# Optimization experiments

Hardware: AMD Instinct MI355X
Metric: run time of the kernel (lower is better)

## Reference

```python
import jax, jax.numpy as jnp
import numpy as np

N = 64   # SSM state size
H = 256  # channels
B = 8    # batch
L = 1024 # sequence length


def setup_inputs() -> dict:
    key = jax.random.key(0)
    k1, k2, k3, k4, k5 = jax.random.split(key, 5)
    scale = 1.0 / np.sqrt(N)  # lecun_normal std for fan_in=N
    inp = jax.random.normal(k1, (B, L, H), jnp.float32)
    As = jax.random.normal(k2, (H, N, N), jnp.float32) * scale
    Bs = jax.random.normal(k3, (H, N, 1), jnp.float32) * scale
    Cs = jax.random.normal(k4, (H, 1, N), jnp.float32) * scale
    Ds = jnp.ones((H,), jnp.float32)
    # log_step_initializer: uniform in [log(dt_min), log(dt_max)]
    lo, hi = np.log(0.001), np.log(0.003)
    log_steps = jax.random.uniform(k5, (H,), jnp.float32) * (hi - lo) + lo
    return {"inp": inp, "As": As, "Bs": Bs, "Cs": Cs, "Ds": Ds, "log_steps": log_steps}


def _discretize(A, B_, C, step):
    # Bilinear (Tustin) discretization, batched over H. step: (H,)
    I = jnp.eye(A.shape[-1], dtype=A.dtype)
    s = (step / 2.0)[:, None, None]            # (H,1,1)
    lhs = I - s * A                            # (H,N,N)
    Ab = jnp.linalg.solve(lhs, I + s * A)      # (H,N,N)
    Bb = jnp.linalg.solve(lhs, (2.0 * s) * B_) # (H,N,1)
    return Ab, Bb, C


def _kernel(Ab, Bb, Cb, length):
    # K[l] = Cb @ Ab^l @ Bb, built via a scan over matrix powers (all heads batched)
    def body(x, _):
        k = jnp.einsum('hon,hno->h', Cb, x)          # (H,)
        x_next = jnp.einsum('hmn,hno->hmo', Ab, x)   # (H,N,1)
        return x_next, k
    _, K = jax.lax.scan(body, Bb, None, length=length)
    return K  # (L, H)


def reference(inp, As, Bs, Cs, Ds, log_steps):
    Lseq = inp.shape[1]
    step = jnp.exp(log_steps)
    Ab, Bb, Cb = _discretize(As, Bs, Cs, step)
    K = _kernel(Ab, Bb, Cb, Lseq)                      # (L, H)
    # causal (non-circular) convolution via FFT, per channel
    n = 2 * Lseq
    Uf = jnp.fft.rfft(inp, n=n, axis=1)                # (B, F, H)
    Kf = jnp.fft.rfft(K, n=n, axis=0)[None]            # (1, F, H)
    y = jnp.fft.irfft(Uf * Kf, n=n, axis=1)[:, :Lseq]  # (B, L, H)
    return y + Ds[None, None, :] * inp
```

## Files before the change

kernel.cpp:

```cpp
#include <hip/hip_runtime.h>
#include <cstddef>

#define SSM_N 64
#define SSM_H 256
#define SSM_B 8
#define SSM_L 1024
#define PAD   68
#define CPAD  65

__device__ __forceinline__ void mat_acc16(const float* Arow, const float* Bmat,
                                          int j0, float acc[16])
{
    #pragma unroll 4
    for (int k = 0; k < SSM_N; ++k) {
        const float a = Arow[k];
        const float4* bp = reinterpret_cast<const float4*>(Bmat + k * PAD + j0);
        const float4 b0 = bp[0];
        const float4 b1 = bp[1];
        const float4 b2 = bp[2];
        const float4 b3 = bp[3];
        acc[0]  += a * b0.x; acc[1]  += a * b0.y; acc[2]  += a * b0.z; acc[3]  += a * b0.w;
        acc[4]  += a * b1.x; acc[5]  += a * b1.y; acc[6]  += a * b1.z; acc[7]  += a * b1.w;
        acc[8]  += a * b2.x; acc[9]  += a * b2.y; acc[10] += a * b2.z; acc[11] += a * b2.w;
        acc[12] += a * b3.x; acc[13] += a * b3.y; acc[14] += a * b3.z; acc[15] += a * b3.w;
    }
}

__global__ __launch_bounds__(256) void ssm_prep_kernel(
    const float* __restrict__ As, const float* __restrict__ Bsin,
    const float* __restrict__ Csin, const float* __restrict__ logsteps,
    float* __restrict__ Kout)
{
    __shared__ __align__(16) float MB[SSM_N * PAD];
    __shared__ __align__(16) float TB[SSM_N * PAD];
    __shared__ float CallL[32 * CPAD];
    __shared__ float XallL[32 * CPAD];
    __shared__ float pbuf[4 * 64];
    __shared__ float bvec[64];

    const int h    = blockIdx.x;
    const int tid  = threadIdx.x;
    const int lane = tid & 63;
    const int q    = tid >> 6;
    const int j0   = q * 16;

    const float step = expf(logsteps[h]);
    const float s    = 0.5f * step;

    const float* Ah = As + (size_t)h * SSM_N * SSM_N;
    #pragma unroll
    for (int r = 0; r < 16; ++r) {
        int e = r * 256 + tid;
        MB[(e >> 6) * PAD + (e & 63)] = s * Ah[e];
    }
    __syncthreads();

    for (int it = 0; it < 3; ++it) {
        float acc[16];
        #pragma unroll
        for (int jj = 0; jj < 16; ++jj) acc[jj] = 0.f;
        const float* Bop = (it == 0) ? MB : TB;
        mat_acc16(MB + lane * PAD, Bop, j0, acc);
        const float4* mp = reinterpret_cast<const float4*>(MB + lane * PAD + j0);
        const float4 m0 = mp[0], m1 = mp[1], m2 = mp[2], m3 = mp[3];
        acc[0]  += m0.x; acc[1]  += m0.y; acc[2]  += m0.z; acc[3]  += m0.w;
        acc[4]  += m1.x; acc[5]  += m1.y; acc[6]  += m1.z; acc[7]  += m1.w;
        acc[8]  += m2.x; acc[9]  += m2.y; acc[10] += m2.z; acc[11] += m2.w;
        acc[12] += m3.x; acc[13] += m3.y; acc[14] += m3.z; acc[15] += m3.w;
        float4* wp = reinterpret_cast<float4*>(TB + lane * PAD + j0);
        wp[0] = make_float4(acc[0],  acc[1],  acc[2],  acc[3]);
        wp[1] = make_float4(acc[4],  acc[5],  acc[6],  acc[7]);
        wp[2] = make_float4(acc[8],  acc[9],  acc[10], acc[11]);
        wp[3] = make_float4(acc[12], acc[13], acc[14], acc[15]);
    }
    __syncthreads();

    #pragma unroll
    for (int r = 0; r < 16; ++r) {
        int e = r * 256 + tid;
        int i = e >> 6, j = e & 63;
        MB[j * PAD + i] = 2.f * TB[i * PAD + j] + ((i == j) ? 1.f : 0.f);
    }
    if (q == 0) {
        pbuf[lane] = Bsin[h * SSM_N + lane];
        float accb = 0.f;
        #pragma unroll 4
        for (int k = 0; k < SSM_N; ++k)
            accb += TB[lane * PAD + k] * pbuf[k];
        bvec[lane] = step * (pbuf[lane] + accb);
    } else if (q == 1) {
        CallL[lane] = Csin[h * SSM_N + lane];
    }
    __syncthreads();

    for (int j = 0; j < 31; ++j) {
        const float* crow = CallL + j * CPAD;
        float p = 0.f;
        #pragma unroll
        for (int kk = 0; kk < 16; ++kk) {
            int k = j0 + kk;
            p += crow[k] * TB[k * PAD + lane];
        }
        pbuf[q * 64 + lane] = p;
        __syncthreads();
        if (q == 0) {
            CallL[(j + 1) * CPAD + lane] =
                crow[lane] + 2.f * (pbuf[lane] + pbuf[64 + lane] + pbuf[128 + lane] + pbuf[192 + lane]);
        }
        __syncthreads();
    }

    {
        float* src = MB;
        float* dst = TB;
        for (int it = 0; it < 5; ++it) {
            float acc[16];
            #pragma unroll
            for (int jj = 0; jj < 16; ++jj) acc[jj] = 0.f;
            mat_acc16(src + lane * PAD, src, j0, acc);
            float4* wp = reinterpret_cast<float4*>(dst + lane * PAD + j0);
            wp[0] = make_float4(acc[0],  acc[1],  acc[2],  acc[3]);
            wp[1] = make_float4(acc[4],  acc[5],  acc[6],  acc[7]);
            wp[2] = make_float4(acc[8],  acc[9],  acc[10], acc[11]);
            wp[3] = make_float4(acc[12], acc[13], acc[14], acc[15]);
            __syncthreads();
            float* tmp = src; src = dst; dst = tmp;
        }
    }

    if (q == 0) XallL[lane] = bvec[lane];
    __syncthreads();
    for (int m = 0; m < 31; ++m) {
        const float* xrow = XallL + m * CPAD;
        float p = 0.f;
        #pragma unroll
        for (int kk = 0; kk < 16; ++kk) {
            int k = j0 + kk;
            p += xrow[k] * TB[k * PAD + lane];
        }
        pbuf[q * 64 + lane] = p;
        __syncthreads();
        if (q == 0)
            XallL[(m + 1) * CPAD + lane] =
                pbuf[lane] + pbuf[64 + lane] + pbuf[128 + lane] + pbuf[192 + lane];
        __syncthreads();
    }

    #pragma unroll
    for (int r = 0; r < 4; ++r) {
        int l  = r * 256 + tid;
        int mm = l >> 5, jj = l & 31;
        const float* cr = CallL + jj * CPAD;
        const float* xr = XallL + mm * CPAD;
        float sacc = 0.f;
        #pragma unroll 4
        for (int i = 0; i < SSM_N; ++i) sacc += cr[i] * xr[i];
        Kout[(size_t)l * SSM_H + h] = sacc;
    }
}

__global__ __launch_bounds__(256) void ssm_conv_kernel(
    const float* __restrict__ U, const float* __restrict__ Kk,
    const float* __restrict__ Ds, float* __restrict__ Y)
{
    const int h = threadIdx.x;
    const int b = blockIdx.x & 7;
    const int p = blockIdx.x >> 3;
    const float dh = Ds[h];
    const float* Ub = U + (size_t)b * SSM_L * SSM_H + h;
    float* Yb = Y + (size_t)b * SSM_L * SSM_H + h;

    #pragma unroll
    for (int half = 0; half < 2; ++half) {
        const int t  = (half == 0) ? p : (63 - p);
        const int l0 = t << 4;
        const int nd = l0 + 16;
        float acc[16], uw[16], u0[16];
        #pragma unroll
        for (int i = 0; i < 16; ++i) {
            float v = Ub[(l0 + i) * SSM_H];
            acc[i] = 0.f; uw[i] = v; u0[i] = v;
        }
        for (int d0 = 0; d0 < nd; d0 += 16) {
            #pragma unroll
            for (int dd = 0; dd < 16; ++dd) {
                const int d = d0 + dd;
                const float kv = Kk[d * SSM_H + h];
                #pragma unroll
                for (int i = 0; i < 16; ++i) acc[i] += kv * uw[i];
                const int li = l0 - 1 - d;
                const float nu = (li >= 0) ? Ub[li * SSM_H] : 0.f;
                #pragma unroll
                for (int i = 15; i > 0; --i) uw[i] = uw[i - 1];
                uw[0] = nu;
            }
        }
        #pragma unroll
        for (int i = 0; i < 16; ++i)
            Yb[(l0 + i) * SSM_H] = acc[i] + dh * u0[i];
    }
}

extern "C" void kernel_launch(void* const* d_in, const int* in_sizes, int n_in,
                              void* d_out, int out_size, void* d_ws, size_t ws_size,
                              hipStream_t stream)
{
    const float* inp     = (const float*)d_in[0];
    const float* As      = (const float*)d_in[1];
    const float* Bsin    = (const float*)d_in[2];
    const float* Csin    = (const float*)d_in[3];
    const float* Dsin    = (const float*)d_in[4];
    const float* lsteps  = (const float*)d_in[5];
    float* Y    = (float*)d_out;
    float* Kbuf = (float*)d_ws;

    ssm_prep_kernel<<<dim3(SSM_H), dim3(256), 0, stream>>>(As, Bsin, Csin, lsteps, Kbuf);
    ssm_conv_kernel<<<dim3(SSM_B * 32), dim3(256), 0, stream>>>(inp, Kbuf, Dsin, Y);
}
```

Baseline: 181.6 us.

## Restructure prep matmuls with register rows and retile conv to 8-row tiles

```diff
diff --git a/kernel.cpp b/kernel.cpp
--- a/kernel.cpp
+++ b/kernel.cpp
@@ -5,38 +5,19 @@
 #define SSM_H 256
 #define SSM_B 8
 #define SSM_L 1024
-#define PAD   68
-#define CPAD  65
-
-__device__ __forceinline__ void mat_acc16(const float* Arow, const float* Bmat,
-                                          int j0, float acc[16])
-{
-    #pragma unroll 4
-    for (int k = 0; k < SSM_N; ++k) {
-        const float a = Arow[k];
-        const float4* bp = reinterpret_cast<const float4*>(Bmat + k * PAD + j0);
-        const float4 b0 = bp[0];
-        const float4 b1 = bp[1];
-        const float4 b2 = bp[2];
-        const float4 b3 = bp[3];
-        acc[0]  += a * b0.x; acc[1]  += a * b0.y; acc[2]  += a * b0.z; acc[3]  += a * b0.w;
-        acc[4]  += a * b1.x; acc[5]  += a * b1.y; acc[6]  += a * b1.z; acc[7]  += a * b1.w;
-        acc[8]  += a * b2.x; acc[9]  += a * b2.y; acc[10] += a * b2.z; acc[11] += a * b2.w;
-        acc[12] += a * b3.x; acc[13] += a * b3.y; acc[14] += a * b3.z; acc[15] += a * b3.w;
-    }
-}
+#define PADM  68
+#define PADC  68
 
 __global__ __launch_bounds__(256) void ssm_prep_kernel(
     const float* __restrict__ As, const float* __restrict__ Bsin,
     const float* __restrict__ Csin, const float* __restrict__ logsteps,
     float* __restrict__ Kout)
 {
-    __shared__ __align__(16) float MB[SSM_N * PAD];
-    __shared__ __align__(16) float TB[SSM_N * PAD];
-    __shared__ float CallL[32 * CPAD];
-    __shared__ float XallL[32 * CPAD];
+    __shared__ __align__(16) float B0[SSM_N * PADM];
+    __shared__ __align__(16) float B1[SSM_N * PADM];
+    __shared__ __align__(16) float CallL[32 * PADC];
+    __shared__ __align__(16) float XallL[32 * PADC];
     __shared__ float pbuf[4 * 64];
-    __shared__ float bvec[64];
 
     const int h    = blockIdx.x;
     const int tid  = threadIdx.x;
@@ -47,27 +28,41 @@
     const float step = expf(logsteps[h]);
     const float s    = 0.5f * step;
 
-    const float* Ah = As + (size_t)h * SSM_N * SSM_N;
-    #pragma unroll
-    for (int r = 0; r < 16; ++r) {
-        int e = r * 256 + tid;
-        MB[(e >> 6) * PAD + (e & 63)] = s * Ah[e];
-    }
-    __syncthreads();
-
-    for (int it = 0; it < 3; ++it) {
+    float arow[64];
+    {
+        const float4* Ar = reinterpret_cast<const float4*>(As + (size_t)h * 4096 + lane * 64);
+        #pragma unroll
+        for (int r = 0; r < 16; ++r) {
+            float4 v = Ar[r];
+            arow[4*r+0] = s * v.x; arow[4*r+1] = s * v.y;
+            arow[4*r+2] = s * v.z; arow[4*r+3] = s * v.w;
+        }
+        if (q == 0) {
+            float4* wp = reinterpret_cast<float4*>(B1 + lane * PADM);
+            #pragma unroll
+            for (int r = 0; r < 16; ++r)
+                wp[r] = make_float4(arow[4*r], arow[4*r+1], arow[4*r+2], arow[4*r+3]);
+        }
+    }
+    __syncthreads();
+
+    #pragma unroll 1
+    for (int it = 0; it < 2; ++it) {
+        const float* Bop = (it == 0) ? B1 : B0;
         float acc[16];
         #pragma unroll
-        for (int jj = 0; jj < 16; ++jj) acc[jj] = 0.f;
-        const float* Bop = (it == 0) ? MB : TB;
-        mat_acc16(MB + lane * PAD, Bop, j0, acc);
-        const float4* mp = reinterpret_cast<const float4*>(MB + lane * PAD + j0);
-        const float4 m0 = mp[0], m1 = mp[1], m2 = mp[2], m3 = mp[3];
-        acc[0]  += m0.x; acc[1]  += m0.y; acc[2]  += m0.z; acc[3]  += m0.w;
-        acc[4]  += m1.x; acc[5]  += m1.y; acc[6]  += m1.z; acc[7]  += m1.w;
-        acc[8]  += m2.x; acc[9]  += m2.y; acc[10] += m2.z; acc[11] += m2.w;
-        acc[12] += m3.x; acc[13] += m3.y; acc[14] += m3.z; acc[15] += m3.w;
-        float4* wp = reinterpret_cast<float4*>(TB + lane * PAD + j0);
+        for (int jj = 0; jj < 16; ++jj) acc[jj] = arow[j0 + jj];
+        #pragma unroll
+        for (int k = 0; k < 64; ++k) {
+            const float a = arow[k];
+            const float4* bp = reinterpret_cast<const float4*>(Bop + k * PADM + j0);
+            const float4 b0 = bp[0], b1v = bp[1], b2 = bp[2], b3 = bp[3];
+            acc[0]  += a * b0.x;  acc[1]  += a * b0.y;  acc[2]  += a * b0.z;  acc[3]  += a * b0.w;
+            acc[4]  += a * b1v.x; acc[5]  += a * b1v.y; acc[6]  += a * b1v.z; acc[7]  += a * b1v.w;
+            acc[8]  += a * b2.x;  acc[9]  += a * b2.y;  acc[10] += a * b2.z;  acc[11] += a * b2.w;
+            acc[12] += a * b3.x;  acc[13] += a * b3.y;  acc[14] += a * b3.z;  acc[15] += a * b3.w;
+        }
+        float4* wp = reinterpret_cast<float4*>(B0 + lane * PADM + j0);
         wp[0] = make_float4(acc[0],  acc[1],  acc[2],  acc[3]);
         wp[1] = make_float4(acc[4],  acc[5],  acc[6],  acc[7]);
         wp[2] = make_float4(acc[8],  acc[9],  acc[10], acc[11]);
@@ -75,50 +70,67 @@
     }
     __syncthreads();
 
+    if (q == 0)      pbuf[lane]  = Bsin[h * SSM_N + lane];
+    else if (q == 1) CallL[lane] = Csin[h * SSM_N + lane];
     #pragma unroll
     for (int r = 0; r < 16; ++r) {
-        int e = r * 256 + tid;
-        int i = e >> 6, j = e & 63;
-        MB[j * PAD + i] = 2.f * TB[i * PAD + j] + ((i == j) ? 1.f : 0.f);
-    }
+        int e = r * 256 + tid, i = e >> 6, j = e & 63;
+        B1[j * PADM + i] = 2.f * B0[i * PADM + j] + ((i == j) ? 1.f : 0.f);
+    }
+    __syncthreads();
+
     if (q == 0) {
-        pbuf[lane] = Bsin[h * SSM_N + lane];
         float accb = 0.f;
-        #pragma unroll 4
-        for (int k = 0; k < SSM_N; ++k)
-            accb += TB[lane * PAD + k] * pbuf[k];
-        bvec[lane] = step * (pbuf[lane] + accb);
-    } else if (q == 1) {
-        CallL[lane] = Csin[h * SSM_N + lane];
-    }
-    __syncthreads();
-
+        #pragma unroll
+        for (int r = 0; r < 16; ++r) {
+            const float4 sv = *reinterpret_cast<const float4*>(B0 + lane * PADM + 4 * r);
+            accb += sv.x * pbuf[4*r] + sv.y * pbuf[4*r+1] + sv.z * pbuf[4*r+2] + sv.w * pbuf[4*r+3];
+        }
+        XallL[lane] = step * (pbuf[lane] + accb);
+    }
+
+    #pragma unroll 1
     for (int j = 0; j < 31; ++j) {
-        const float* crow = CallL + j * CPAD;
-        float p = 0.f;
-        #pragma unroll
-        for (int kk = 0; kk < 16; ++kk) {
-            int k = j0 + kk;
-            p += crow[k] * TB[k * PAD + lane];
-        }
-        pbuf[q * 64 + lane] = p;
-        __syncthreads();
-        if (q == 0) {
-            CallL[(j + 1) * CPAD + lane] =
-                crow[lane] + 2.f * (pbuf[lane] + pbuf[64 + lane] + pbuf[128 + lane] + pbuf[192 + lane]);
-        }
+        const float* crow = CallL + j * PADC;
+        float pp = 0.f;
+        #pragma unroll
+        for (int r = 0; r < 4; ++r) {
+            const float4 cc = *reinterpret_cast<const float4*>(crow + j0 + 4 * r);
+            const float4 aa = *reinterpret_cast<const float4*>(B1 + lane * PADM + j0 + 4 * r);
+            pp += cc.x * aa.x + cc.y * aa.y + cc.z * aa.z + cc.w * aa.w;
+        }
+        pbuf[q * 64 + lane] = pp;
+        __syncthreads();
+        if (q == 0)
+            CallL[(j + 1) * PADC + lane] =
+                pbuf[lane] + pbuf[64 + lane] + pbuf[128 + lane] + pbuf[192 + lane];
         __syncthreads();
     }
 
     {
-        float* src = MB;
-        float* dst = TB;
+        float* src = B1;
+        float* dst = B0;
+        #pragma unroll 1
         for (int it = 0; it < 5; ++it) {
+            #pragma unroll
+            for (int r = 0; r < 16; ++r) {
+                const float4 v = *reinterpret_cast<const float4*>(src + lane * PADM + 4 * r);
+                arow[4*r] = v.x; arow[4*r+1] = v.y; arow[4*r+2] = v.z; arow[4*r+3] = v.w;
+            }
             float acc[16];
             #pragma unroll
             for (int jj = 0; jj < 16; ++jj) acc[jj] = 0.f;
-            mat_acc16(src + lane * PAD, src, j0, acc);
-            float4* wp = reinterpret_cast<float4*>(dst + lane * PAD + j0);
+            #pragma unroll
+            for (int k = 0; k < 64; ++k) {
+                const float a = arow[k];
+                const float4* bp = reinterpret_cast<const float4*>(src + k * PADM + j0);
+                const float4 b0 = bp[0], b1v = bp[1], b2 = bp[2], b3 = bp[3];
+                acc[0]  += a * b0.x;  acc[1]  += a * b0.y;  acc[2]  += a * b0.z;  acc[3]  += a * b0.w;
+                acc[4]  += a * b1v.x; acc[5]  += a * b1v.y; acc[6]  += a * b1v.z; acc[7]  += a * b1v.w;
+                acc[8]  += a * b2.x;  acc[9]  += a * b2.y;  acc[10] += a * b2.z;  acc[11] += a * b2.w;
+                acc[12] += a * b3.x;  acc[13] += a * b3.y;  acc[14] += a * b3.z;  acc[15] += a * b3.w;
+            }
+            float4* wp = reinterpret_cast<float4*>(dst + lane * PADM + j0);
             wp[0] = make_float4(acc[0],  acc[1],  acc[2],  acc[3]);
             wp[1] = make_float4(acc[4],  acc[5],  acc[6],  acc[7]);
             wp[2] = make_float4(acc[8],  acc[9],  acc[10], acc[11]);
@@ -128,33 +140,42 @@
         }
     }
 
-    if (q == 0) XallL[lane] = bvec[lane];
-    __syncthreads();
+    #pragma unroll
+    for (int r = 0; r < 16; ++r) {
+        int e = r * 256 + tid, i = e >> 6, jj = e & 63;
+        B1[i * PADM + jj] = B0[jj * PADM + i];
+    }
+    __syncthreads();
+
+    #pragma unroll 1
     for (int m = 0; m < 31; ++m) {
-        const float* xrow = XallL + m * CPAD;
-        float p = 0.f;
-        #pragma unroll
-        for (int kk = 0; kk < 16; ++kk) {
-            int k = j0 + kk;
-            p += xrow[k] * TB[k * PAD + lane];
-        }
-        pbuf[q * 64 + lane] = p;
+        const float* xrow = XallL + m * PADC;
+        float pp = 0.f;
+        #pragma unroll
+        for (int r = 0; r < 4; ++r) {
+            const float4 xx = *reinterpret_cast<const float4*>(xrow + j0 + 4 * r);
+            const float4 aa = *reinterpret_cast<const float4*>(B1 + lane * PADM + j0 + 4 * r);
+            pp += xx.x * aa.x + xx.y * aa.y + xx.z * aa.z + xx.w * aa.w;
+        }
+        pbuf[q * 64 + lane] = pp;
         __syncthreads();
         if (q == 0)
-            XallL[(m + 1) * CPAD + lane] =
+            XallL[(m + 1) * PADC + lane] =
                 pbuf[lane] + pbuf[64 + lane] + pbuf[128 + lane] + pbuf[192 + lane];
         __syncthreads();
     }
 
     #pragma unroll
     for (int r = 0; r < 4; ++r) {
-        int l  = r * 256 + tid;
-        int mm = l >> 5, jj = l & 31;
-        const float* cr = CallL + jj * CPAD;
-        const float* xr = XallL + mm * CPAD;
+        int l = r * 256 + tid, mm = l >> 5, jj = l & 31;
+        const float4* cr = reinterpret_cast<const float4*>(CallL + jj * PADC);
+        const float4* xr = reinterpret_cast<const float4*>(XallL + mm * PADC);
         float sacc = 0.f;
-        #pragma unroll 4
-        for (int i = 0; i < SSM_N; ++i) sacc += cr[i] * xr[i];
+        #pragma unroll
+        for (int i = 0; i < 16; ++i) {
+            const float4 c4 = cr[i], x4 = xr[i];
+            sacc += c4.x * x4.x + c4.y * x4.y + c4.z * x4.z + c4.w * x4.w;
+        }
         Kout[(size_t)l * SSM_H + h] = sacc;
     }
 }
@@ -172,31 +193,46 @@
 
     #pragma unroll
     for (int half = 0; half < 2; ++half) {
-        const int t  = (half == 0) ? p : (63 - p);
-        const int l0 = t << 4;
-        const int nd = l0 + 16;
-        float acc[16], uw[16], u0[16];
-        #pragma unroll
-        for (int i = 0; i < 16; ++i) {
-            float v = Ub[(l0 + i) * SSM_H];
-            acc[i] = 0.f; uw[i] = v; u0[i] = v;
-        }
-        for (int d0 = 0; d0 < nd; d0 += 16) {
-            #pragma unroll
-            for (int dd = 0; dd < 16; ++dd) {
-                const int d = d0 + dd;
-                const float kv = Kk[d * SSM_H + h];
+        const int t  = (half == 0) ? p : (127 - p);
+        const int l0 = t << 3;
+        const int nd = l0 + 8;
+        float acc[8], win[15], kreg[8], u0[8];
+
+        #pragma unroll
+        for (int j = 0; j < 15; ++j) {
+            const int li = l0 - 7 + j;
+            win[j] = (li >= 0) ? Ub[li * SSM_H] : 0.f;
+        }
+        #pragma unroll
+        for (int i = 0; i < 8; ++i) { acc[i] = 0.f; u0[i] = win[7 + i]; }
+        #pragma unroll
+        for (int j = 0; j < 8; ++j) kreg[j] = Kk[j * SSM_H + h];
+
+        for (int d0 = 0; d0 < nd; d0 += 8) {
+            float kn[8], nw[8];
+            const int dn = d0 + 8;
+            #pragma unroll
+            for (int j = 0; j < 8; ++j)
+                kn[j] = (dn + j < nd) ? Kk[(dn + j) * SSM_H + h] : 0.f;
+            #pragma unroll
+            for (int j = 0; j < 8; ++j) {
+                const int li = l0 - d0 - 15 + j;
+                nw[j] = (li >= 0) ? Ub[li * SSM_H] : 0.f;
+            }
+            #pragma unroll
+            for (int dd = 0; dd < 8; ++dd) {
+                const float kv = kreg[dd];
                 #pragma unroll
-                for (int i = 0; i < 16; ++i) acc[i] += kv * uw[i];
-                const int li = l0 - 1 - d;
-                const float nu = (li >= 0) ? Ub[li * SSM_H] : 0.f;
-                #pragma unroll
-                for (int i = 15; i > 0; --i) uw[i] = uw[i - 1];
-                uw[0] = nu;
-            }
-        }
-        #pragma unroll
-        for (int i = 0; i < 16; ++i)
+                for (int i = 0; i < 8; ++i)
+                    acc[i] += kv * win[7 + i - dd];
+            }
+            #pragma unroll
+            for (int j = 14; j >= 8; --j) win[j] = win[j - 8];
+            #pragma unroll
+            for (int j = 0; j < 8; ++j) { win[j] = nw[j]; kreg[j] = kn[j]; }
+        }
+        #pragma unroll
+        for (int i = 0; i < 8; ++i)
             Yb[(l0 + i) * SSM_H] = acc[i] + dh * u0[i];
     }
 }
@@ -205,15 +241,15 @@
                               void* d_out, int out_size, void* d_ws, size_t ws_size,
                               hipStream_t stream)
 {
-    const float* inp     = (const float*)d_in[0];
-    const float* As      = (const float*)d_in[1];
-    const float* Bsin    = (const float*)d_in[2];
-    const float* Csin    = (const float*)d_in[3];
-    const float* Dsin    = (const float*)d_in[4];
-    const float* lsteps  = (const float*)d_in[5];
+    const float* inp    = (const float*)d_in[0];
+    const float* As     = (const float*)d_in[1];
+    const float* Bsin   = (const float*)d_in[2];
+    const float* Csin   = (const float*)d_in[3];
+    const float* Dsin   = (const float*)d_in[4];
+    const float* lsteps = (const float*)d_in[5];
     float* Y    = (float*)d_out;
     float* Kbuf = (float*)d_ws;
 
     ssm_prep_kernel<<<dim3(SSM_H), dim3(256), 0, stream>>>(As, Bsin, Csin, lsteps, Kbuf);
-    ssm_conv_kernel<<<dim3(SSM_B * 32), dim3(256), 0, stream>>>(inp, Kbuf, Dsin, Y);
+    ssm_conv_kernel<<<dim3(SSM_B * 16 * 4), dim3(256), 0, stream>>>(inp, Kbuf, Dsin, Y);
 }
```

After: 237.5 us. 1.31x slower.
